# Kernel tuning notes

Measured on AMD Instinct MI355X. Metric: run time of the kernel, lower is better.

The kernel has to match this reference:

```python
import jax, jax.numpy as jnp
import numpy as np

TOP_K = 2


def setup_inputs() -> dict:
    key = jax.random.key(0)
    k1, k2 = jax.random.split(key)
    hidden_states = jax.random.normal(k1, (4, 8192, 4096), dtype=jnp.float32)
    weight = jax.random.normal(k2, (64, 4096), dtype=jnp.float32) * 0.02
    return {"hidden_states": hidden_states, "weight": weight}


def reference(hidden_states, weight):
    bsz, seq_len, h = hidden_states.shape
    x = hidden_states.reshape(-1, h)                      # [T, h]
    logits = jnp.einsum('th,eh->te', x, weight)           # [T, E] router logits
    scores = jax.nn.softmax(logits, axis=-1)
    topk_weight, topk_idx = jax.lax.top_k(scores, TOP_K)  # [T, k] each
    # norm_topk_prob is False in the module, so no renormalization.
    return topk_idx, topk_weight
```

## Files before the change

### kernel.cpp

```cpp
#include <hip/hip_runtime.h>
#include <math.h>


#define BK 64

__device__ __forceinline__ void gl_lds16(const float* g, float* l) {
  __builtin_amdgcn_global_load_lds(
      (const __attribute__((address_space(1))) unsigned int*)g,
      (__attribute__((address_space(3))) unsigned int*)l,
      16, 0, 0);
}

__global__ __launch_bounds__(256)
void moe_gate(const float* __restrict__ X, const float* __restrict__ W,
              float* __restrict__ out, int T) {
  __shared__ float smem[8192];
  float* sx = smem;
  float* sw = smem + 4096;

  const int t    = threadIdx.x;
  const int lane = t & 63;
  const int wave = t >> 6;
  const int tr   = t & 15;
  const int tc   = t >> 4;
  const long tok0 = (long)blockIdx.x * 64;

  const float* xg[4];
  const float* wg[4];
  float* ldx[4];
  float* ldw[4];
  {
    const int rl = lane >> 4;
    const int c4 = lane & 15;
    #pragma unroll
    for (int i = 0; i < 4; ++i) {
      const int r  = wave * 16 + i * 4 + rl;
      const int sz = (wave * 4 + i) & 15;
      const int gc = c4 ^ sz;
      xg[i] = X + (tok0 + r) * 4096 + gc * 4;
      wg[i] = W + (long)r * 4096 + gc * 4;
      ldx[i] = sx + (wave * 16 + i * 4) * 64;
      ldw[i] = sw + (wave * 16 + i * 4) * 64;
    }
  }

  float acc[4][4];
  #pragma unroll
  for (int i = 0; i < 4; ++i)
    #pragma unroll
    for (int j = 0; j < 4; ++j) acc[i][j] = 0.f;

  for (int k0 = 0; k0 < 4096; k0 += BK) {
    #pragma unroll
    for (int i = 0; i < 4; ++i) {
      gl_lds16(xg[i] + k0, ldx[i]);
      gl_lds16(wg[i] + k0, ldw[i]);
    }
    __syncthreads();

    float cacc[4][4];
    #pragma unroll
    for (int i = 0; i < 4; ++i)
      #pragma unroll
      for (int j = 0; j < 4; ++j) cacc[i][j] = 0.f;

    #pragma unroll
    for (int k4 = 0; k4 < 16; ++k4) {
      float4 xa[4], wb[4];
      #pragma unroll
      for (int i = 0; i < 4; ++i) {
        const int row  = tr * 4 + i;
        const int slot = k4 ^ (row >> 2);
        xa[i] = *(const float4*)(sx + row * 64 + slot * 4);
      }
      #pragma unroll
      for (int j = 0; j < 4; ++j) {
        const int e    = tc * 4 + j;
        const int slot = k4 ^ (e >> 2);
        wb[j] = *(const float4*)(sw + e * 64 + slot * 4);
      }
      #pragma unroll
      for (int i = 0; i < 4; ++i)
        #pragma unroll
        for (int j = 0; j < 4; ++j) {
          cacc[i][j] = fmaf(xa[i].x, wb[j].x, cacc[i][j]);
          cacc[i][j] = fmaf(xa[i].y, wb[j].y, cacc[i][j]);
          cacc[i][j] = fmaf(xa[i].z, wb[j].z, cacc[i][j]);
          cacc[i][j] = fmaf(xa[i].w, wb[j].w, cacc[i][j]);
        }
    }
    #pragma unroll
    for (int i = 0; i < 4; ++i)
      #pragma unroll
      for (int j = 0; j < 4; ++j) acc[i][j] += cacc[i][j];
    __syncthreads();
  }

  #pragma unroll
  for (int i = 0; i < 4; ++i)
    #pragma unroll
    for (int j = 0; j < 4; ++j)
      smem[(tr * 4 + i) * 65 + tc * 4 + j] = acc[i][j];
  __syncthreads();

  if (t < 64) {
    const float* row = smem + t * 65;
    float b1 = -1e30f, b2 = -1e30f;
    int i1 = 0, i2 = 0;
    for (int e = 0; e < 64; ++e) {
      const float v = row[e];
      if (v > b1)      { b2 = b1; i2 = i1; b1 = v; i1 = e; }
      else if (v > b2) { b2 = v; i2 = e; }
    }
    float s = 0.f;
    for (int e = 0; e < 64; ++e) s += expf(row[e] - b1);
    const float inv = 1.0f / s;
    const long gt = tok0 + t;
    out[gt * 2 + 0] = (float)i1;
    out[gt * 2 + 1] = (float)i2;
    float* ow = out + (long)T * 2;
    ow[gt * 2 + 0] = inv;
    ow[gt * 2 + 1] = expf(b2 - b1) * inv;
  }
}

extern "C" void kernel_launch(void* const* d_in, const int* in_sizes, int n_in,
                              void* d_out, int out_size, void* d_ws, size_t ws_size,
                              hipStream_t stream) {
  const float* X = (const float*)d_in[0];
  const float* W = (const float*)d_in[1];
  float* out = (float*)d_out;
  const int T = in_sizes[0] / 4096;
  const int grid = T / 64;
  hipLaunchKernelGGL(moe_gate, dim3(grid), dim3(256), 0, stream, X, W, out, T);
}
```

Before: 829.4 us.

## Double-buffer LDS tiles to overlap global loads with FMA compute

Doubles shared memory to two 8192-float buffers and prefetches the next K-chunk of X and W into the alternate buffer while computing on the current one. This drops to one barrier per iteration. It also simplifies the swizzled LDS index math using precomputed float4 base pointers and XOR on tr/tc. The larger LDS footprint (64KB) may lower occupancy per CU.

```diff
diff --git a/kernel.cpp b/kernel.cpp
--- a/kernel.cpp
+++ b/kernel.cpp
@@ -1,8 +1,6 @@
 #include <hip/hip_runtime.h>
 #include <math.h>
 
-
-#define BK 64
 
 __device__ __forceinline__ void gl_lds16(const float* g, float* l) {
   __builtin_amdgcn_global_load_lds(
@@ -14,9 +12,7 @@
 __global__ __launch_bounds__(256)
 void moe_gate(const float* __restrict__ X, const float* __restrict__ W,
               float* __restrict__ out, int T) {
-  __shared__ float smem[8192];
-  float* sx = smem;
-  float* sw = smem + 4096;
+  __shared__ float smem[16384];
 
   const int t    = threadIdx.x;
   const int lane = t & 63;
@@ -27,8 +23,7 @@
 
   const float* xg[4];
   const float* wg[4];
-  float* ldx[4];
-  float* ldw[4];
+  int lofs[4];
   {
     const int rl = lane >> 4;
     const int c4 = lane & 15;
@@ -39,8 +34,7 @@
       const int gc = c4 ^ sz;
       xg[i] = X + (tok0 + r) * 4096 + gc * 4;
       wg[i] = W + (long)r * 4096 + gc * 4;
-      ldx[i] = sx + (wave * 16 + i * 4) * 64;
-      ldw[i] = sw + (wave * 16 + i * 4) * 64;
+      lofs[i] = (wave * 16 + i * 4) * 64;
     }
   }
 
@@ -50,13 +44,28 @@
     #pragma unroll
     for (int j = 0; j < 4; ++j) acc[i][j] = 0.f;
 
-  for (int k0 = 0; k0 < 4096; k0 += BK) {
-    #pragma unroll
-    for (int i = 0; i < 4; ++i) {
-      gl_lds16(xg[i] + k0, ldx[i]);
-      gl_lds16(wg[i] + k0, ldw[i]);
+  #pragma unroll
+  for (int i = 0; i < 4; ++i) {
+    gl_lds16(xg[i], smem + lofs[i]);
+    gl_lds16(wg[i], smem + 4096 + lofs[i]);
+  }
+
+  for (int c = 0; c < 64; ++c) {
+    __syncthreads();
+    const int cur = c & 1;
+    if (c + 1 < 64) {
+      const int nxt = cur ^ 1;
+      float* dst = smem + nxt * 8192;
+      const long k0 = (long)(c + 1) * 64;
+      #pragma unroll
+      for (int i = 0; i < 4; ++i) {
+        gl_lds16(xg[i] + k0, dst + lofs[i]);
+        gl_lds16(wg[i] + k0, dst + 4096 + lofs[i]);
+      }
     }
-    __syncthreads();
+
+    const float4* xb = (const float4*)(smem + cur * 8192) + tr * 64;
+    const float4* wb4 = (const float4*)(smem + cur * 8192 + 4096) + tc * 64;
 
     float cacc[4][4];
     #pragma unroll
@@ -66,19 +75,13 @@
 
     #pragma unroll
     for (int k4 = 0; k4 < 16; ++k4) {
+      const int sx4 = k4 ^ tr;
+      const int sw4 = k4 ^ tc;
       float4 xa[4], wb[4];
       #pragma unroll
-      for (int i = 0; i < 4; ++i) {
-        const int row  = tr * 4 + i;
-        const int slot = k4 ^ (row >> 2);
-        xa[i] = *(const float4*)(sx + row * 64 + slot * 4);
-      }
+      for (int i = 0; i < 4; ++i) xa[i] = xb[i * 16 + sx4];
       #pragma unroll
-      for (int j = 0; j < 4; ++j) {
-        const int e    = tc * 4 + j;
-        const int slot = k4 ^ (e >> 2);
-        wb[j] = *(const float4*)(sw + e * 64 + slot * 4);
-      }
+      for (int j = 0; j < 4; ++j) wb[j] = wb4[j * 16 + sw4];
       #pragma unroll
       for (int i = 0; i < 4; ++i)
         #pragma unroll
@@ -93,7 +96,6 @@
     for (int i = 0; i < 4; ++i)
       #pragma unroll
       for (int j = 0; j < 4; ++j) acc[i][j] += cacc[i][j];
-    __syncthreads();
   }
 
   #pragma unroll
```

Result: no change. 835.9 us (+0.8%).
